# Performance work log

Hardware: AMD Instinct MI355X
Metric: run time of the kernel (lower is better)

Reference implementation:

```python
import jax, jax.numpy as jnp
import numpy as np
from jax import lax

B, L, C = 8, 1024, 256
H = 8  # num_heads
EPS = 1e-5


def _conv_bn(img, w, gamma, beta):
    # img: [B, C_in, h, w]; w: [C_out, C_in, 3, 3]; 3x3 conv, stride 1, pad 1, no bias
    out = lax.conv_general_dilated(img, w, window_strides=(1, 1),
                                   padding=[(1, 1), (1, 1)],
                                   dimension_numbers=('NCHW', 'OIHW', 'NCHW'))
    # BatchNorm2d in train mode: per-channel batch stats over (B, h, w), biased var
    mu = out.mean(axis=(0, 2, 3), keepdims=True)
    var = out.var(axis=(0, 2, 3), keepdims=True)
    out = (out - mu) * lax.rsqrt(var + EPS)
    out = out * gamma[None, :, None, None] + beta[None, :, None, None]
    b, c, hh, ww = out.shape
    return out.reshape(b, c, hh * ww).transpose(0, 2, 1)  # b (h w) c


def setup_inputs() -> dict:
    key = jax.random.key(0)
    ks = jax.random.split(key, 10)
    s = 0.02
    inp = {
        'x': jax.random.normal(ks[0], (B, L, C), jnp.float32),
        'y': jax.random.normal(ks[1], (B, L, C), jnp.float32),
        'h': 32,
        'w': 32,
        'conv_q_w': jax.random.normal(ks[2], (C, C, 3, 3), jnp.float32) * s,
        'bn_q_g': jnp.ones((C,), jnp.float32),
        'bn_q_b': jnp.zeros((C,), jnp.float32),
        'conv_k_w': jax.random.normal(ks[3], (C, C, 3, 3), jnp.float32) * s,
        'bn_k_g': jnp.ones((C,), jnp.float32),
        'bn_k_b': jnp.zeros((C,), jnp.float32),
        'conv_v_w': jax.random.normal(ks[4], (C, C, 3, 3), jnp.float32) * s,
        'bn_v_g': jnp.ones((C,), jnp.float32),
        'bn_v_b': jnp.zeros((C,), jnp.float32),
        'Wq': jax.random.normal(ks[5], (C, C), jnp.float32) * s,
        'Wk': jax.random.normal(ks[6], (C, C), jnp.float32) * s,
        'Wv': jax.random.normal(ks[7], (C, C), jnp.float32) * s,
        'Wo': jax.random.normal(ks[8], (C, C), jnp.float32) * s,
        'bo': jnp.zeros((C,), jnp.float32),
    }
    return inp


def reference(x, y, h, w,
              conv_q_w, bn_q_g, bn_q_b,
              conv_k_w, bn_k_g, bn_k_b,
              conv_v_w, bn_v_g, bn_v_b,
              Wq, Wk, Wv, Wo, bo):
    b, t, c = x.shape
    x_img = x.transpose(0, 2, 1).reshape(b, c, h, w)
    y_img = y.transpose(0, 2, 1).reshape(b, c, h, w)

    q = _conv_bn(x_img, conv_q_w, bn_q_g, bn_q_b)  # [B, L, C]
    k = _conv_bn(y_img, conv_k_w, bn_k_g, bn_k_b)
    v = _conv_bn(y_img, conv_v_w, bn_v_g, bn_v_b)

    d = c // H
    # Linear (no bias) then split heads: b t (h d) -> b h t d
    q = (q @ Wq.T).reshape(b, -1, H, d).transpose(0, 2, 1, 3)
    k = (k @ Wk.T).reshape(b, -1, H, d).transpose(0, 2, 1, 3)
    v = (v @ Wv.T).reshape(b, -1, H, d).transpose(0, 2, 1, 3)

    scale = c ** (-0.5)  # NOTE: original scales by dim_q**-0.5, not head_dim
    attn = jax.nn.softmax(jnp.einsum('bhlk,bhtk->bhlt', q, k) * scale, axis=-1)
    out = jnp.einsum('bhlt,bhtv->bhlv', attn, v)
    out = out.transpose(0, 2, 1, 3).reshape(b, -1, c)  # b h t d -> b t (h d)
    return out @ Wo.T + bo
```

## Files before the change

### kernel.cpp

```cpp
#include <hip/hip_runtime.h>
#include <cmath>

#define BB 8
#define LLEN 1024
#define CC 256
#define NH 8
#define HD 32
#define IMG 32
#define EPSBN 1e-5f
#define QSCALE 0.0625f
#define SCLOG2E 0.09016844005556f

typedef short bf16x8 __attribute__((ext_vector_type(8)));
typedef short bf16x4 __attribute__((ext_vector_type(4)));
typedef float f32x4 __attribute__((ext_vector_type(4)));

static __device__ __forceinline__ unsigned short f2bf(float v) {
  union { float f; unsigned u; } a; a.f = v;
  unsigned r = a.u + 0x7fff + ((a.u >> 16) & 1);
  return (unsigned short)(r >> 16);
}
static __device__ __forceinline__ float bf2f(unsigned short s) {
  union { unsigned u; float f; } a; a.u = ((unsigned)s) << 16; return a.f;
}

__global__ __launch_bounds__(256) void k_prep(const float* __restrict__ x,
                                              const float* __restrict__ y,
                                              const float* __restrict__ w0,
                                              const float* __restrict__ w1,
                                              const float* __restrict__ w2,
                                              const float* __restrict__ Wo,
                                              short* __restrict__ xh,
                                              short* __restrict__ yh,
                                              short* __restrict__ Wp,
                                              short* __restrict__ Woh,
                                              short* __restrict__ Wol) {
  int bid = blockIdx.x;
  if (bid < 4096) {
    const float* s = bid >= 2048 ? y : x;
    short* d = bid >= 2048 ? yh : xh;
    size_t i = (size_t)((bid & 2047) << 8) + threadIdx.x;
    float4 v = ((const float4*)s)[i];
    bf16x4 o;
    o[0] = (short)f2bf(v.x); o[1] = (short)f2bf(v.y);
    o[2] = (short)f2bf(v.z); o[3] = (short)f2bf(v.w);
    *(bf16x4*)(d + i * 4) = o;
  } else if (bid < 4864) {
    int k = bid - 4096;
    int t = k >> 8, co = k & 255, ci = threadIdx.x;
    const float* w = t == 0 ? w0 : (t == 1 ? w1 : w2);
    const float* src = w + ((size_t)co * CC + ci) * 9;
    int cb = co >> 6, nt = (co >> 4) & 3, mmw = co & 15;
    int kcw = ci >> 5, quadw = (ci >> 3) & 3, e = ci & 7;
    int lanew = quadw * 16 + mmw;
    size_t base = ((size_t)(t * 4 + cb) * 8 + kcw) * 9;
#pragma unroll
    for (int tap = 0; tap < 9; ++tap)
      Wp[((base + tap) * 4 + nt) * 512 + lanew * 8 + e] = (short)f2bf(src[tap]);
  } else {
    int i = ((bid - 4864) << 8) + threadIdx.x;
    float v = Wo[i];
    unsigned short h = f2bf(v);
    Woh[i] = (short)h;
    Wol[i] = (short)f2bf(v - bf2f(h));
  }
}

__global__ __launch_bounds__(256, 3) void k_conv(const short* __restrict__ xh,
                                                 const short* __restrict__ yh,
                                                 const short* __restrict__ Wp,
                                                 short* __restrict__ ch,
                                                 float* __restrict__ st) {
  __shared__ __align__(16) short sI[2][204 * 32];
  __shared__ float sws[4][32];
  __shared__ float swq[4][32];

  int tid = threadIdx.x;
  int cb = blockIdx.x;
  int co0 = cb << 6;
  int r0 = blockIdx.y << 2;
  int z = blockIdx.z;
  int t = z >> 3, b = z & 7;
  const short* inb = (t == 0 ? xh : yh) + (size_t)b * LLEN * CC;

  int lane = tid & 63, w = tid >> 6;
  int quad = lane >> 4, mm = lane & 15;
  int wr = w & 1, wc = w >> 1;

  int pbA[4];
#pragma unroll
  for (int mt = 0; mt < 4; ++mt) {
    int sp = wr * 64 + mt * 16 + mm;
    pbA[mt] = (sp >> 5) * 34 + (sp & 31);
  }
  const int dtap[9] = {0, 1, 2, 34, 35, 36, 68, 69, 70};

  bool ivalid[4], iact[4];
  int ioff[4], sidx[4];
#pragma unroll
  for (int j = 0; j < 4; ++j) {
    int idx = tid + (j << 8);
    ivalid[j] = idx < 816;
    int sp_p = idx >> 2, cg = idx & 3;
    int pr = sp_p / 34;
    int px = sp_p - pr * 34;
    int ir = r0 - 1 + pr;
    int xx = px - 1;
    iact[j] = ivalid[j] && (ir >= 0) && (ir < IMG) && (xx >= 0) && (xx < IMG);
    ioff[j] = ((ir < 0 ? 0 : ir) * 32 + (xx < 0 ? 0 : (xx > 31 ? 31 : xx))) * CC + cg * 8;
    sidx[j] = sp_p * 32 + (((cg + (sp_p >> 1)) & 3) << 3);
  }

  const short* wlane = Wp + ((size_t)(t * 4 + cb) * 8 * 9 * 4) * 512 + lane * 8;

  f32x4 acc[4][2];
#pragma unroll
  for (int mt = 0; mt < 4; ++mt)
#pragma unroll
    for (int nt = 0; nt < 2; ++nt) acc[mt][nt] = (f32x4){0.f, 0.f, 0.f, 0.f};

  bf16x8 zerov = {0, 0, 0, 0, 0, 0, 0, 0};
  bf16x8 ipf[4];
#pragma unroll
  for (int j = 0; j < 4; ++j)
    ipf[j] = iact[j] ? *(const bf16x8*)(inb + ioff[j]) : zerov;

  bf16x8 Bw[4][2];
#pragma unroll
  for (int f = 0; f < 3; ++f)
#pragma unroll
    for (int nt = 0; nt < 2; ++nt)
      Bw[f][nt] = *(const bf16x8*)(wlane + (size_t)(f * 4 + wc * 2 + nt) * 512);

#pragma unroll
  for (int j = 0; j < 4; ++j)
    if (ivalid[j]) *(bf16x8*)(sI[0] + sidx[j]) = ipf[j];
  __syncthreads();

#pragma unroll
  for (int kc = 0; kc < 8; ++kc) {
    if (kc < 7) {
#pragma unroll
      for (int j = 0; j < 4; ++j)
        ipf[j] = iact[j] ? *(const bf16x8*)(inb + ioff[j] + ((kc + 1) << 5)) : zerov;
    }
    const short* sc = sI[kc & 1];

#pragma unroll
    for (int tap = 0; tap < 9; ++tap) {
      const int f = kc * 9 + tap;
      if (f + 3 < 72) {
        const int nf = f + 3;
#pragma unroll
        for (int nt = 0; nt < 2; ++nt)
          Bw[nf & 3][nt] =
              *(const bf16x8*)(wlane + (size_t)(nf * 4 + wc * 2 + nt) * 512);
      }
      bf16x8 Af[4];
#pragma unroll
      for (int mt = 0; mt < 4; ++mt) {
        int sp_p = pbA[mt] + dtap[tap];
        Af[mt] = *(const bf16x8*)(sc + sp_p * 32 + (((quad + (sp_p >> 1)) & 3) << 3));
      }
#pragma unroll
      for (int mt = 0; mt < 4; ++mt)
#pragma unroll
        for (int nt = 0; nt < 2; ++nt)
          acc[mt][nt] = __builtin_amdgcn_mfma_f32_16x16x32_bf16(Af[mt], Bw[f & 3][nt],
                                                                acc[mt][nt], 0, 0, 0);
    }

    if (kc < 7) {
#pragma unroll
      for (int j = 0; j < 4; ++j)
        if (ivalid[j]) *(bf16x8*)(sI[(kc + 1) & 1] + sidx[j]) = ipf[j];
      __syncthreads();
    }
  }

  size_t tb = (size_t)t * 8192 + b * 1024 + r0 * 32;
#pragma unroll
  for (int mt = 0; mt < 4; ++mt)
#pragma unroll
    for (int nt = 0; nt < 2; ++nt)
#pragma unroll
      for (int r = 0; r < 4; ++r) {
        int sp = wr * 64 + mt * 16 + quad * 4 + r;
        ch[(tb + sp) * CC + co0 + wc * 32 + nt * 16 + mm] = (short)f2bf(acc[mt][nt][r]);
      }

  float s[2], q[2];
#pragma unroll
  for (int nt = 0; nt < 2; ++nt) {
    float ss = 0.f, qq = 0.f;
#pragma unroll
    for (int mt = 0; mt < 4; ++mt)
#pragma unroll
      for (int r = 0; r < 4; ++r) {
        float v = acc[mt][nt][r];
        ss += v;
        qq += v * v;
      }
    ss += __shfl_xor(ss, 16); ss += __shfl_xor(ss, 32);
    qq += __shfl_xor(qq, 16); qq += __shfl_xor(qq, 32);
    s[nt] = ss; q[nt] = qq;
  }
  if (quad == 0) {
#pragma unroll
    for (int nt = 0; nt < 2; ++nt) {
      sws[w][nt * 16 + mm] = s[nt];
      swq[w][nt * 16 + mm] = q[nt];
    }
  }
  __syncthreads();
  if (tid < 64) {
    int wcr = tid >> 5, cl = tid & 31;
    float S = sws[wcr * 2 + 0][cl] + sws[wcr * 2 + 1][cl];
    float Q = swq[wcr * 2 + 0][cl] + swq[wcr * 2 + 1][cl];
    atomicAdd(&st[t * 512 + co0 + tid], S);
    atomicAdd(&st[t * 512 + 256 + co0 + tid], Q);
  }
}

__global__ __launch_bounds__(256) void k_fuse(const float* __restrict__ Wq,
                                              const float* __restrict__ Wk,
                                              const float* __restrict__ Wv,
                                              const float* __restrict__ gq,
                                              const float* __restrict__ gk,
                                              const float* __restrict__ gv,
                                              const float* __restrict__ bq,
                                              const float* __restrict__ bk,
                                              const float* __restrict__ bv,
                                              const float* __restrict__ st,
                                              short* __restrict__ Wfh,
                                              short* __restrict__ Wfl,
                                              float* __restrict__ bfv) {
  int t = blockIdx.y;
  const float* W = t == 0 ? Wq : (t == 1 ? Wk : Wv);
  const float* gamma = t == 0 ? gq : (t == 1 ? gk : gv);
  const float* beta = t == 0 ? bq : (t == 1 ? bk : bv);
  int co = blockIdx.x, ci = threadIdx.x;
  float mu = st[t * 512 + ci] * (1.f / 8192.f);
  float var = st[t * 512 + 256 + ci] * (1.f / 8192.f) - mu * mu;
  float a = gamma[ci] * rsqrtf(var + EPSBN);
  float dt = beta[ci] - mu * a;
  float wv = W[co * CC + ci];
  float v = wv * a;
  unsigned short hh = f2bf(v);
  Wfh[(size_t)t * 65536 + co * CC + ci] = (short)hh;
  Wfl[(size_t)t * 65536 + co * CC + ci] = (short)f2bf(v - bf2f(hh));
  __shared__ float red[256];
  red[ci] = dt * wv;
  __syncthreads();
  for (int s2 = 128; s2 > 0; s2 >>= 1) {
    if (ci < s2) red[ci] += red[ci + s2];
    __syncthreads();
  }
  if (ci == 0) bfv[t * 256 + co] = red[0];
}

__global__ __launch_bounds__(256, 2) void k_proj(const short* __restrict__ ch,
                                                 const short* __restrict__ Wfh,
                                                 const short* __restrict__ Wfl,
                                                 const float* __restrict__ bfv,
                                                 short* __restrict__ Qh,
                                                 short* __restrict__ Kh,
                                                 short* __restrict__ Vh) {
  __shared__ __align__(16) short sT[64 * 136];
  int tid = threadIdx.x;
  int t = blockIdx.z;
  int t0 = blockIdx.x << 7;
  int co0 = blockIdx.y << 6;
  int lane = tid & 63, w = tid >> 6;
  int quad = lane >> 4, mm = lane & 15;
  int colw = co0 + w * 16;
  const short* cht = ch + (size_t)t * 8192 * CC;

  bf16x8 Bh[8], Bl[8];
  {
    const short* bh = Wfh + (size_t)t * 65536 + (size_t)(colw + mm) * CC + quad * 8;
    const short* bl = Wfl + (size_t)t * 65536 + (size_t)(colw + mm) * CC + quad * 8;
#pragma unroll
    for (int kc = 0; kc < 8; ++kc) {
      Bh[kc] = *(const bf16x8*)(bh + kc * 32);
      Bl[kc] = *(const bf16x8*)(bl + kc * 32);
    }
  }
  float bv = bfv[t * 256 + colw + mm];

  int c = colw + mm;
  int hh = c >> 5, dd = c & 31;
  int bb = t0 >> 10, lbase = t0 & 1023;
  size_t hb = (size_t)(bb * 8 + hh) * 1024;

  bf16x8 A0[8], A1[8];
  auto loadA = [&](bf16x8* dst, int g) {
    const short* a = cht + (size_t)(t0 + g * 16 + mm) * CC + quad * 8;
#pragma unroll
    for (int kc = 0; kc < 8; ++kc) dst[kc] = *(const bf16x8*)(a + kc * 32);
  };
  auto compute = [&](const bf16x8* A, int g) {
    f32x4 aH = {0.f, 0.f, 0.f, 0.f}, aL = {0.f, 0.f, 0.f, 0.f};
#pragma unroll
    for (int kc = 0; kc < 8; ++kc) {
      aH = __builtin_amdgcn_mfma_f32_16x16x32_bf16(A[kc], Bh[kc], aH, 0, 0, 0);
      aL = __builtin_amdgcn_mfma_f32_16x16x32_bf16(A[kc], Bl[kc], aL, 0, 0, 0);
    }
    if (t == 0) {
#pragma unroll
      for (int r = 0; r < 4; ++r) {
        int l = lbase + g * 16 + quad * 4 + r;
        Qh[(hb + l) * 32 + dd] = (short)f2bf((aH[r] + aL[r] + bv) * SCLOG2E);
      }
    } else if (t == 1) {
#pragma unroll
      for (int r = 0; r < 4; ++r) {
        int l = lbase + g * 16 + quad * 4 + r;
        Kh[(hb + l) * 32 + dd] = (short)f2bf(aH[r] + aL[r] + bv);
      }
    } else {
#pragma unroll
      for (int r = 0; r < 4; ++r)
        sT[(w * 16 + mm) * 136 + (g >> 2) * 64 + 16 * quad + 4 * r + (g & 3)] =
            (short)f2bf(aH[r] + aL[r] + bv);
    }
  };

  loadA(A0, 0);
#pragma unroll
  for (int g = 0; g < 8; g += 2) {
    loadA(A1, g + 1);
    compute(A0, g);
    if (g + 2 < 8) loadA(A0, g + 2);
    compute(A1, g + 1);
  }

  if (t == 2) {
    __syncthreads();
    int b = t0 >> 10, l0 = t0 & 1023;
#pragma unroll
    for (int j = 0; j < 4; ++j) {
      int idx = tid + (j << 8);
      int co = idx >> 4, tg = idx & 15;
      bf16x8 v = *(const bf16x8*)(sT + co * 136 + tg * 8);
      *(bf16x8*)(Vh + ((size_t)(b * CC) + co0 + co) * LLEN + l0 + tg * 8) = v;
    }
  }
}

__global__ __launch_bounds__(256, 2) void k_attn(const short* __restrict__ Qh,
                                                 const short* __restrict__ Kh,
                                                 const short* __restrict__ Vh,
                                                 short* __restrict__ AOh) {
  __shared__ __align__(16) short sK[2][64 * 40];
  __shared__ __align__(16) short sV[2][32 * 72];
  __shared__ __align__(16) short sP[4 * 32 * 72];

  int tid = threadIdx.x;
  int lane = tid & 63, w = tid >> 6;
  int quad = lane >> 4, mm = lane & 15;
  int bh = blockIdx.x;
  int b = bh >> 3, h = bh & 7;
  int l0 = blockIdx.y << 7;

  bf16x8 qf[2];
#pragma unroll
  for (int mf = 0; mf < 2; ++mf)
    qf[mf] = *(const bf16x8*)(Qh + ((size_t)bh * 1024 + l0 + w * 32 + mf * 16 + mm) * 32 +
                              quad * 8);

  f32x4 accO[2][2], accL[2];
#pragma unroll
  for (int mf = 0; mf < 2; ++mf) {
    accO[mf][0] = (f32x4){0.f, 0.f, 0.f, 0.f};
    accO[mf][1] = (f32x4){0.f, 0.f, 0.f, 0.f};
    accL[mf] = (f32x4){0.f, 0.f, 0.f, 0.f};
  }
  bf16x8 ones;
#pragma unroll
  for (int j = 0; j < 8; ++j) ones[j] = (short)0x3F80;

  int kt = tid >> 2, kc4 = tid & 3;
  const short* kgp = Kh + ((size_t)bh * 1024 + kt) * 32 + kc4 * 8;
  int kofs = kt * 40 + kc4 * 8;
  int vd = tid >> 3, vt8 = tid & 7;
  const short* vgp = Vh + ((size_t)(b * CC) + h * HD + vd) * LLEN + vt8 * 8;
  int vofs = vd * 72 + vt8 * 8;
  short* pw = sP + w * (32 * 72);

  bf16x8 kr = *(const bf16x8*)kgp;
  bf16x8 vr = *(const bf16x8*)vgp;
  *(bf16x8*)(sK[0] + kofs) = kr;
  *(bf16x8*)(sV[0] + vofs) = vr;
  __syncthreads();

  for (int tt = 0; tt < 16; ++tt) {
    if (tt < 15) {
      kr = *(const bf16x8*)(kgp + (size_t)(tt + 1) * 64 * 32);
      vr = *(const bf16x8*)(vgp + (tt + 1) * 64);
    }
    const short* sKc = sK[tt & 1];
    const short* sVc = sV[tt & 1];

#pragma unroll
    for (int mf = 0; mf < 2; ++mf) {
      f32x4 accS[4];
#pragma unroll
      for (int nt = 0; nt < 4; ++nt) {
        bf16x8 kf = *(const bf16x8*)(sKc + (nt * 16 + mm) * 40 + quad * 8);
        f32x4 z = {0.f, 0.f, 0.f, 0.f};
        accS[nt] = __builtin_amdgcn_mfma_f32_16x16x32_bf16(qf[mf], kf, z, 0, 0, 0);
      }
#pragma unroll
      for (int r = 0; r < 4; ++r) {
        int q = mf * 16 + quad * 4 + r;
        bf16x4 pk;
#pragma unroll
        for (int nt = 0; nt < 4; ++nt) {
          union { float f; unsigned u; } cv;
          cv.f = __builtin_exp2f(accS[nt][r]);
          pk[nt] = (short)((cv.u + 0x8000u) >> 16);
        }
        *(bf16x4*)(pw + q * 72 + mm * 4) = pk;
      }
    }

#pragma unroll
    for (int kc = 0; kc < 2; ++kc) {
      bf16x8 vf0 = *(const bf16x8*)(sVc + mm * 72 + kc * 32 + quad * 8);
      bf16x8 vf1 = *(const bf16x8*)(sVc + (16 + mm) * 72 + kc * 32 + quad * 8);
#pragma unroll
      for (int mf = 0; mf < 2; ++mf) {
        bf16x8 pf = *(const bf16x8*)(pw + (mf * 16 + mm) * 72 + kc * 32 + quad * 8);
        accL[mf] = __builtin_amdgcn_mfma_f32_16x16x32_bf16(pf, ones, accL[mf], 0, 0, 0);
        accO[mf][0] = __builtin_amdgcn_mfma_f32_16x16x32_bf16(pf, vf0, accO[mf][0], 0, 0, 0);
        accO[mf][1] = __builtin_amdgcn_mfma_f32_16x16x32_bf16(pf, vf1, accO[mf][1], 0, 0, 0);
      }
    }

    if (tt < 15) {
      __syncthreads();
      *(bf16x8*)(sK[(tt + 1) & 1] + kofs) = kr;
      *(bf16x8*)(sV[(tt + 1) & 1] + vofs) = vr;
      __syncthreads();
    }
  }

#pragma unroll
  for (int mf = 0; mf < 2; ++mf)
#pragma unroll
    for (int r = 0; r < 4; ++r) {
      float inv = __builtin_amdgcn_rcpf(accL[mf][r]);
      size_t token = (size_t)(b * LLEN) + l0 + w * 32 + mf * 16 + quad * 4 + r;
      AOh[token * CC + h * HD + mm] = (short)f2bf(accO[mf][0][r] * inv);
      AOh[token * CC + h * HD + 16 + mm] = (short)f2bf(accO[mf][1][r] * inv);
    }
}

__global__ __launch_bounds__(256, 2) void k_out(const short* __restrict__ AOh,
                                                const short* __restrict__ Woh,
                                                const short* __restrict__ Wol,
                                                const float* __restrict__ bo,
                                                float* __restrict__ out) {
  int tid = threadIdx.x;
  int t0 = blockIdx.x << 6;
  int co0 = blockIdx.y << 6;
  int lane = tid & 63, w = tid >> 6;
  int quad = lane >> 4, mm = lane & 15;
  int colw = co0 + w * 16;

  bf16x8 Bh[8], Bl[8];
  {
    const short* bh = Woh + (size_t)(colw + mm) * CC + quad * 8;
    const short* bl = Wol + (size_t)(colw + mm) * CC + quad * 8;
#pragma unroll
    for (int kc = 0; kc < 8; ++kc) {
      Bh[kc] = *(const bf16x8*)(bh + kc * 32);
      Bl[kc] = *(const bf16x8*)(bl + kc * 32);
    }
  }
  float bv = bo[colw + mm];

  bf16x8 A0[8], A1[8];
  auto loadA = [&](bf16x8* dst, int g) {
    const short* a = AOh + (size_t)(t0 + g * 16 + mm) * CC + quad * 8;
#pragma unroll
    for (int kc = 0; kc < 8; ++kc) dst[kc] = *(const bf16x8*)(a + kc * 32);
  };
  auto compute = [&](const bf16x8* A, int g) {
    f32x4 aH = {0.f, 0.f, 0.f, 0.f}, aL = {0.f, 0.f, 0.f, 0.f};
#pragma unroll
    for (int kc = 0; kc < 8; ++kc) {
      aH = __builtin_amdgcn_mfma_f32_16x16x32_bf16(A[kc], Bh[kc], aH, 0, 0, 0);
      aL = __builtin_amdgcn_mfma_f32_16x16x32_bf16(A[kc], Bl[kc], aL, 0, 0, 0);
    }
#pragma unroll
    for (int r = 0; r < 4; ++r) {
      int token = t0 + g * 16 + quad * 4 + r;
      out[(size_t)token * CC + colw + mm] = aH[r] + aL[r] + bv;
    }
  };

  loadA(A0, 0);
#pragma unroll
  for (int g = 0; g < 4; g += 2) {
    loadA(A1, g + 1);
    compute(A0, g);
    if (g + 2 < 4) loadA(A0, g + 2);
    compute(A1, g + 1);
  }
}

extern "C" void kernel_launch(void* const* d_in, const int* in_sizes, int n_in,
                              void* d_out, int out_size, void* d_ws, size_t ws_size,
                              hipStream_t stream) {
  (void)in_sizes; (void)n_in; (void)out_size; (void)ws_size;
  const float* x  = (const float*)d_in[0];
  const float* y  = (const float*)d_in[1];
  const float* wq = (const float*)d_in[4];
  const float* gq = (const float*)d_in[5];
  const float* bq = (const float*)d_in[6];
  const float* wk = (const float*)d_in[7];
  const float* gk = (const float*)d_in[8];
  const float* bk = (const float*)d_in[9];
  const float* wv = (const float*)d_in[10];
  const float* gv = (const float*)d_in[11];
  const float* bv = (const float*)d_in[12];
  const float* Wq = (const float*)d_in[13];
  const float* Wk = (const float*)d_in[14];
  const float* Wv = (const float*)d_in[15];
  const float* Wo = (const float*)d_in[16];
  const float* bo = (const float*)d_in[17];
  float* out = (float*)d_out;

  const size_t NP = (size_t)8192 * 256;
  short* xh  = (short*)d_ws;
  short* yh  = xh + NP;
  short* ch  = yh + NP;
  short* Qh  = ch + 3 * NP;
  short* Kh  = Qh + NP;
  short* Vh  = Kh + NP;
  short* AOh = Vh + NP;
  short* Wp  = AOh + NP;
  short* Wfh = Wp + (size_t)3 * 9 * 65536;
  short* Wfl = Wfh + 3 * 65536;
  short* Woh = Wfl + 3 * 65536;
  short* Wol = Woh + 65536;
  float* st  = (float*)(Wol + 65536);
  float* bfv = st + 1536;

  hipMemsetAsync(st, 0, 1536 * sizeof(float), stream);

  k_prep<<<5120, 256, 0, stream>>>(x, y, wq, wk, wv, Wo, xh, yh, Wp, Woh, Wol);

  k_conv<<<dim3(4, 8, 24), 256, 0, stream>>>(xh, yh, Wp, ch, st);

  k_fuse<<<dim3(256, 3), 256, 0, stream>>>(Wq, Wk, Wv, gq, gk, gv, bq, bk, bv,
                                           st, Wfh, Wfl, bfv);

  k_proj<<<dim3(64, 4, 3), 256, 0, stream>>>(ch, Wfh, Wfl, bfv, Qh, Kh, Vh);

  k_attn<<<dim3(64, 8), 256, 0, stream>>>(Qh, Kh, Vh, AOh);

  k_out<<<dim3(128, 4), 256, 0, stream>>>(AOh, Woh, Wol, bo, out);
}
```

Before: 207.5 us.

## Fold BN-weight fusion into projection kernel and zero stats in prep

Removes the separate k_fuse kernel by having each k_proj block compute the BN scale/shift from the stats and build its split bf16 hi/lo weight fragments and bias directly from the fp32 weights. The hipMemsetAsync of the stats buffer is replaced by zeroing inside k_prep, cutting two launches. It also drops one __syncthreads in the attention double-buffer loop. The cost is that every projection block redoes the weight scaling and bias reduction, and removing that barrier may open a race on the shared K/V buffers.

```diff
diff --git a/kernel.cpp b/kernel.cpp
--- a/kernel.cpp
+++ b/kernel.cpp
@@ -34,7 +34,8 @@
                                               short* __restrict__ yh,
                                               short* __restrict__ Wp,
                                               short* __restrict__ Woh,
-                                              short* __restrict__ Wol) {
+                                              short* __restrict__ Wol,
+                                              float* __restrict__ st) {
   int bid = blockIdx.x;
   if (bid < 4096) {
     const float* s = bid >= 2048 ? y : x;
@@ -58,6 +59,10 @@
     for (int tap = 0; tap < 9; ++tap)
       Wp[((base + tap) * 4 + nt) * 512 + lanew * 8 + e] = (short)f2bf(src[tap]);
   } else {
+    if (bid == 4864) {
+#pragma unroll
+      for (int j = 0; j < 6; ++j) st[threadIdx.x * 6 + j] = 0.f;
+    }
     int i = ((bid - 4864) << 8) + threadIdx.x;
     float v = Wo[i];
     unsigned short h = f2bf(v);
@@ -222,51 +227,22 @@
   }
 }
 
-__global__ __launch_bounds__(256) void k_fuse(const float* __restrict__ Wq,
-                                              const float* __restrict__ Wk,
-                                              const float* __restrict__ Wv,
-                                              const float* __restrict__ gq,
-                                              const float* __restrict__ gk,
-                                              const float* __restrict__ gv,
-                                              const float* __restrict__ bq,
-                                              const float* __restrict__ bk,
-                                              const float* __restrict__ bv,
-                                              const float* __restrict__ st,
-                                              short* __restrict__ Wfh,
-                                              short* __restrict__ Wfl,
-                                              float* __restrict__ bfv) {
-  int t = blockIdx.y;
-  const float* W = t == 0 ? Wq : (t == 1 ? Wk : Wv);
-  const float* gamma = t == 0 ? gq : (t == 1 ? gk : gv);
-  const float* beta = t == 0 ? bq : (t == 1 ? bk : bv);
-  int co = blockIdx.x, ci = threadIdx.x;
-  float mu = st[t * 512 + ci] * (1.f / 8192.f);
-  float var = st[t * 512 + 256 + ci] * (1.f / 8192.f) - mu * mu;
-  float a = gamma[ci] * rsqrtf(var + EPSBN);
-  float dt = beta[ci] - mu * a;
-  float wv = W[co * CC + ci];
-  float v = wv * a;
-  unsigned short hh = f2bf(v);
-  Wfh[(size_t)t * 65536 + co * CC + ci] = (short)hh;
-  Wfl[(size_t)t * 65536 + co * CC + ci] = (short)f2bf(v - bf2f(hh));
-  __shared__ float red[256];
-  red[ci] = dt * wv;
-  __syncthreads();
-  for (int s2 = 128; s2 > 0; s2 >>= 1) {
-    if (ci < s2) red[ci] += red[ci + s2];
-    __syncthreads();
-  }
-  if (ci == 0) bfv[t * 256 + co] = red[0];
-}
-
 __global__ __launch_bounds__(256, 2) void k_proj(const short* __restrict__ ch,
-                                                 const short* __restrict__ Wfh,
-                                                 const short* __restrict__ Wfl,
-                                                 const float* __restrict__ bfv,
+                                                 const float* __restrict__ Wq,
+                                                 const float* __restrict__ Wk,
+                                                 const float* __restrict__ Wv,
+                                                 const float* __restrict__ gq,
+                                                 const float* __restrict__ gk,
+                                                 const float* __restrict__ gv,
+                                                 const float* __restrict__ bq,
+                                                 const float* __restrict__ bk,
+                                                 const float* __restrict__ bv_,
+                                                 const float* __restrict__ st,
                                                  short* __restrict__ Qh,
                                                  short* __restrict__ Kh,
                                                  short* __restrict__ Vh) {
   __shared__ __align__(16) short sT[64 * 136];
+  __shared__ float sa[256], sdt[256];
   int tid = threadIdx.x;
   int t = blockIdx.z;
   int t0 = blockIdx.x << 7;
@@ -276,17 +252,42 @@
   int colw = co0 + w * 16;
   const short* cht = ch + (size_t)t * 8192 * CC;
 
+  const float* W = t == 0 ? Wq : (t == 1 ? Wk : Wv);
+  const float* gamma = t == 0 ? gq : (t == 1 ? gk : gv);
+  const float* beta = t == 0 ? bq : (t == 1 ? bk : bv_);
+
+  {
+    float mu = st[t * 512 + tid] * (1.f / 8192.f);
+    float var = st[t * 512 + 256 + tid] * (1.f / 8192.f) - mu * mu;
+    float a = gamma[tid] * rsqrtf(var + EPSBN);
+    sa[tid] = a;
+    sdt[tid] = beta[tid] - mu * a;
+  }
+  __syncthreads();
+
   bf16x8 Bh[8], Bl[8];
+  float bacc = 0.f;
   {
-    const short* bh = Wfh + (size_t)t * 65536 + (size_t)(colw + mm) * CC + quad * 8;
-    const short* bl = Wfl + (size_t)t * 65536 + (size_t)(colw + mm) * CC + quad * 8;
+    const float* wrow = W + (size_t)(colw + mm) * CC + quad * 8;
 #pragma unroll
     for (int kc = 0; kc < 8; ++kc) {
-      Bh[kc] = *(const bf16x8*)(bh + kc * 32);
-      Bl[kc] = *(const bf16x8*)(bl + kc * 32);
-    }
-  }
-  float bv = bfv[t * 256 + colw + mm];
+      float4 w0 = *(const float4*)(wrow + kc * 32);
+      float4 w1 = *(const float4*)(wrow + kc * 32 + 4);
+      float wv8[8] = {w0.x, w0.y, w0.z, w0.w, w1.x, w1.y, w1.z, w1.w};
+#pragma unroll
+      for (int e = 0; e < 8; ++e) {
+        int ci = kc * 32 + quad * 8 + e;
+        float v = wv8[e] * sa[ci];
+        unsigned short hh2 = f2bf(v);
+        Bh[kc][e] = (short)hh2;
+        Bl[kc][e] = (short)f2bf(v - bf2f(hh2));
+        bacc += sdt[ci] * wv8[e];
+      }
+    }
+  }
+  bacc += __shfl_xor(bacc, 16);
+  bacc += __shfl_xor(bacc, 32);
+  float bv = bacc;
 
   int c = colw + mm;
   int hh = c >> 5, dd = c & 31;
@@ -439,7 +440,6 @@
     }
 
     if (tt < 15) {
-      __syncthreads();
       *(bf16x8*)(sK[(tt + 1) & 1] + kofs) = kr;
       *(bf16x8*)(sV[(tt + 1) & 1] + vofs) = vr;
       __syncthreads();
@@ -542,23 +542,16 @@
   short* Vh  = Kh + NP;
   short* AOh = Vh + NP;
   short* Wp  = AOh + NP;
-  short* Wfh = Wp + (size_t)3 * 9 * 65536;
-  short* Wfl = Wfh + 3 * 65536;
-  short* Woh = Wfl + 3 * 65536;
+  short* Woh = Wp + (size_t)3 * 9 * 65536;
   short* Wol = Woh + 65536;
   float* st  = (float*)(Wol + 65536);
-  float* bfv = st + 1536;
-
-  hipMemsetAsync(st, 0, 1536 * sizeof(float), stream);
-
-  k_prep<<<5120, 256, 0, stream>>>(x, y, wq, wk, wv, Wo, xh, yh, Wp, Woh, Wol);
+
+  k_prep<<<5120, 256, 0, stream>>>(x, y, wq, wk, wv, Wo, xh, yh, Wp, Woh, Wol, st);
 
   k_conv<<<dim3(4, 8, 24), 256, 0, stream>>>(xh, yh, Wp, ch, st);
 
-  k_fuse<<<dim3(256, 3), 256, 0, stream>>>(Wq, Wk, Wv, gq, gk, gv, bq, bk, bv,
-                                           st, Wfh, Wfl, bfv);
-
-  k_proj<<<dim3(64, 4, 3), 256, 0, stream>>>(ch, Wfh, Wfl, bfv, Qh, Kh, Vh);
+  k_proj<<<dim3(64, 4, 3), 256, 0, stream>>>(ch, Wq, Wk, Wv, gq, gk, gv,
+                                             bq, bk, bv, st, Qh, Kh, Vh);
 
   k_attn<<<dim3(64, 8), 256, 0, stream>>>(Qh, Kh, Vh, AOh);
 
```

Measured after the change: 206.3 us, median of 2. About the same (-0.6%).
